# Kernel optimization log

Hardware: AMD Instinct MI355X
Metric: run time of the kernel (lower is better)

The kernel has to match this reference:

```python
import jax, jax.numpy as jnp
import numpy as np

EPS = 1e-12  # torch F.normalize default eps

def _l2norm(x):
    # torch.nn.functional.normalize(x, dim=-1): x / max(||x||_2, eps)
    n = jnp.linalg.norm(x, axis=-1, keepdims=True)
    return x / jnp.maximum(n, EPS)

def setup_inputs() -> dict:
    key = jax.random.key(0)
    ks = jax.random.split(key, 12)
    B, T, D, V, C = 16, 2048, 1024, 32000, 6
    s = 0.02
    text = jax.random.randint(ks[0], (B * T,), 0, V, dtype=jnp.int64)
    offsets = (jnp.arange(B, dtype=jnp.int64) * T)  # uniform-length sequences
    emb = jax.random.normal(ks[1], (V, D), dtype=jnp.float32) * s
    Wq = jax.random.normal(ks[2], (D, D), dtype=jnp.float32) * s
    bq = jnp.zeros((D,), jnp.float32)
    Wk = jax.random.normal(ks[3], (D, D), dtype=jnp.float32) * s
    bk = jnp.zeros((D,), jnp.float32)
    Wv = jax.random.normal(ks[4], (D, D), dtype=jnp.float32) * s
    bv = jnp.zeros((D,), jnp.float32)
    Wfc = jax.random.normal(ks[5], (D, D), dtype=jnp.float32) * s
    bfc = jnp.zeros((D,), jnp.float32)
    Wo = jax.random.normal(ks[6], (C, D), dtype=jnp.float32) * s
    bo = jnp.zeros((C,), jnp.float32)
    return {"text": text, "offsets": offsets, "emb": emb,
            "Wq": Wq, "bq": bq, "Wk": Wk, "bk": bk, "Wv": Wv, "bv": bv,
            "Wfc": Wfc, "bfc": bfc, "Wo": Wo, "bo": bo}

def reference(text, offsets, emb, Wq, bq, Wk, bk, Wv, bv, Wfc, bfc, Wo, bo):
    B = offsets.shape[0]
    T = text.shape[0] // B  # uniform lengths -> pad_sequence == reshape
    D = emb.shape[1]
    tok = text.reshape(B, T)
    x = emb[tok]                                   # [B,T,D]
    q = x @ Wq.T + bq
    k = x @ Wk.T + bk
    v = x @ Wv.T + bv
    scores = jnp.einsum('bqd,bkd->bqk', q, k) / jnp.sqrt(jnp.asarray(D, x.dtype))
    causal = jnp.tril(jnp.ones((T, T), dtype=bool))
    scores = jnp.where(causal[None, :, :], scores, -jnp.inf)
    attn = jax.nn.softmax(scores, axis=-1)
    out = jnp.einsum('bqk,bkd->bqd', attn, v) + x  # residual with embedding
    out = _l2norm(out)
    out = out + (out @ Wfc.T + bfc)                # residual FFN
    out = _l2norm(out)
    last = out[:, -1, :]                           # [B,D]
    return jax.nn.sigmoid(last @ Wo.T + bo)        # [B,num_class]
```

## Files before the change

kernel.cpp:

```cpp
#include <hip/hip_runtime.h>
#include <hip/hip_bf16.h>
#include <math.h>

typedef unsigned short ushort_t;

__device__ __forceinline__ float bf2f(ushort_t u) {
    union { unsigned int i; float f; } v;
    v.i = ((unsigned int)u) << 16;
    return v.f;
}

__device__ __forceinline__ ushort_t f2bf(float f) {
    union { float f; unsigned int i; } v; v.f = f;
    unsigned int lsb = (v.i >> 16) & 1;
    unsigned int r = v.i + 0x7FFF + lsb;
    return (ushort_t)(r >> 16);
}

__device__ __forceinline__ float wave_sum(float acc) {
    #pragma unroll
    for (int off = 32; off >= 1; off >>= 1) acc += __shfl_xor(acc, off, 64);
    return acc;
}

__device__ __forceinline__ void ld8(const void* p, int isbf, size_t i, float* o) {
    if (isbf) {
        uint4 raw = *reinterpret_cast<const uint4*>((const ushort_t*)p + i);
        const ushort_t* pu = reinterpret_cast<const ushort_t*>(&raw);
        #pragma unroll
        for (int k = 0; k < 8; ++k) o[k] = bf2f(pu[k]);
    } else {
        const float4* f = reinterpret_cast<const float4*>((const float*)p + i);
        float4 a = f[0], b = f[1];
        o[0]=a.x; o[1]=a.y; o[2]=a.z; o[3]=a.w;
        o[4]=b.x; o[5]=b.y; o[6]=b.z; o[7]=b.w;
    }
}

__device__ __forceinline__ void ld4(const void* p, int isbf, size_t i, float* o) {
    if (isbf) {
        uint2 raw = *reinterpret_cast<const uint2*>((const ushort_t*)p + i);
        const ushort_t* pu = reinterpret_cast<const ushort_t*>(&raw);
        #pragma unroll
        for (int k = 0; k < 4; ++k) o[k] = bf2f(pu[k]);
    } else {
        float4 a = *reinterpret_cast<const float4*>((const float*)p + i);
        o[0]=a.x; o[1]=a.y; o[2]=a.z; o[3]=a.w;
    }
}

__device__ __forceinline__ float ldS(const void* p, int isbf, size_t i) {
    return isbf ? bf2f(((const ushort_t*)p)[i]) : ((const float*)p)[i];
}

__device__ __forceinline__ int tokAt(const void* text, int isi64, size_t i) {
    return isi64 ? ((const int*)text)[2 * i] : ((const int*)text)[i];
}

__global__ void kD_init(const void* __restrict__ emb, const void* __restrict__ text,
                        int* __restrict__ flags, float* __restrict__ zbuf, int nz) {
    if (blockIdx.x == 0) {
        if (threadIdx.x < 64) {
            const int lane = threadIdx.x;
            ushort_t u = ((const ushort_t*)emb)[2 * lane];
            int e = (u >> 7) & 0xFF;
            unsigned long long mb = __ballot(e >= 0x60 && e <= 0x7E);
            int odd = ((const int*)text)[2 * lane + 1];
            unsigned long long mi = __ballot(odd != 0);
            if (lane == 0) {
                flags[0] = (__popcll(mb) >= 32) ? 1 : 0;
                flags[1] = (__popcll(mi) == 0) ? 1 : 0;
            }
        }
    } else {
        int i = (blockIdx.x - 1) * 256 + threadIdx.x;
        if (i < nz) zbuf[i] = 0.f;
    }
}

__global__ void k1_qx(const void* __restrict__ text, const void* __restrict__ emb,
                      const void* __restrict__ Wq, const void* __restrict__ bq,
                      float* __restrict__ x_last, float* __restrict__ q,
                      const int* __restrict__ flags, int T, int D) {
    const int isbf = flags[0], isi64 = flags[1];
    const int nb = D >> 2;
    const int b = blockIdx.x / nb;
    const int r0 = (blockIdx.x % nb) << 2;
    const int tid = threadIdx.x;
    __shared__ float xl[1024];
    const int tok = tokAt(text, isi64, (size_t)b * T + (T - 1));
    float w4[4];
    for (int dd = tid * 4; dd < D; dd += 1024) {
        ld4(emb, isbf, (size_t)tok * D + dd, w4);
        xl[dd]=w4[0]; xl[dd+1]=w4[1]; xl[dd+2]=w4[2]; xl[dd+3]=w4[3];
        if (r0 == 0) *reinterpret_cast<float4*>(x_last + b * D + dd)
                       = make_float4(w4[0], w4[1], w4[2], w4[3]);
    }
    __syncthreads();
    const int wave = tid >> 6, lane = tid & 63;
    const int i = r0 + wave;
    float acc = 0.f, w[8];
    for (int d0 = lane * 8; d0 < D; d0 += 512) {
        ld8(Wq, isbf, (size_t)i * D + d0, w);
        #pragma unroll
        for (int k = 0; k < 8; ++k) acc += w[k] * xl[d0 + k];
    }
    acc = wave_sum(acc);
    if (lane == 0) q[b * D + i] = acc + ldS(bq, isbf, i);
}

__global__ void k2_c(const float* __restrict__ q, const void* __restrict__ Wk,
                     float* __restrict__ c, const int* __restrict__ flags, int D) {
    const int isbf = flags[0];
    const int ich = D >> 5;
    const int b = blockIdx.x / ich;
    const int i0 = (blockIdx.x % ich) << 5;
    __shared__ float qs[32];
    if (threadIdx.x < 32) qs[threadIdx.x] = q[b * D + i0 + threadIdx.x];
    __syncthreads();
    const int d = threadIdx.x * 4;
    float a0 = 0.f, a1 = 0.f, a2 = 0.f, a3 = 0.f, w[4];
    #pragma unroll 8
    for (int i = 0; i < 32; ++i) {
        const float qv = qs[i];
        ld4(Wk, isbf, (size_t)(i0 + i) * D + d, w);
        a0 += qv * w[0]; a1 += qv * w[1]; a2 += qv * w[2]; a3 += qv * w[3];
    }
    atomicAdd(&c[b * D + d + 0], a0);
    atomicAdd(&c[b * D + d + 1], a1);
    atomicAdd(&c[b * D + d + 2], a2);
    atomicAdd(&c[b * D + d + 3], a3);
}

__global__ void k3_scores(const void* __restrict__ text, const void* __restrict__ emb,
                          const float* __restrict__ c, float* __restrict__ s,
                          const int* __restrict__ flags, int T, int D, float scale) {
    const int isbf = flags[0], isi64 = flags[1];
    const int jb = T >> 2;
    const int b = blockIdx.x / jb;
    const int j0 = (blockIdx.x % jb) * 4;
    __shared__ float cs[1024];
    for (int dd = threadIdx.x * 4; dd < D; dd += 1024) {
        float4 v = *reinterpret_cast<const float4*>(c + b * D + dd);
        cs[dd]=v.x; cs[dd+1]=v.y; cs[dd+2]=v.z; cs[dd+3]=v.w;
    }
    __syncthreads();
    const int wave = threadIdx.x >> 6, lane = threadIdx.x & 63;
    const int j = j0 + wave;
    const int tok = tokAt(text, isi64, (size_t)b * T + j);
    float acc = 0.f, w[8];
    for (int d0 = lane * 8; d0 < D; d0 += 512) {
        ld8(emb, isbf, (size_t)tok * D + d0, w);
        #pragma unroll
        for (int k = 0; k < 8; ++k) acc += w[k] * cs[d0 + k];
    }
    acc = wave_sum(acc);
    if (lane == 0) s[b * T + j] = acc * scale;
}

__global__ void k4_stats(const float* __restrict__ s, float* __restrict__ m,
                         float* __restrict__ l, int T) {
    const int b = blockIdx.x;
    const int tid = threadIdx.x;
    __shared__ float red[256];
    float mx = -INFINITY;
    for (int j = tid; j < T; j += 256) mx = fmaxf(mx, s[b * T + j]);
    red[tid] = mx;
    __syncthreads();
    for (int st = 128; st; st >>= 1) {
        if (tid < st) red[tid] = fmaxf(red[tid], red[tid + st]);
        __syncthreads();
    }
    mx = red[0];
    __syncthreads();
    float sm = 0.f;
    for (int j = tid; j < T; j += 256) sm += expf(s[b * T + j] - mx);
    red[tid] = sm;
    __syncthreads();
    for (int st = 128; st; st >>= 1) {
        if (tid < st) red[tid] += red[tid + st];
        __syncthreads();
    }
    if (tid == 0) { m[b] = mx; l[b] = red[0]; }
}

__global__ void k5_xbar(const void* __restrict__ text, const void* __restrict__ emb,
                        const float* __restrict__ s, const float* __restrict__ m,
                        const float* __restrict__ l, float* __restrict__ xbar,
                        const int* __restrict__ flags, int T, int D) {
    const int isbf = flags[0], isi64 = flags[1];
    const int jc = T >> 5;
    const int b = blockIdx.x / jc;
    const int j0 = (blockIdx.x % jc) << 5;
    const int tid = threadIdx.x;
    __shared__ float wts[32];
    __shared__ int tk[32];
    if (tid < 32) {
        const float mm = m[b], ll = l[b];
        wts[tid] = expf(s[b * T + j0 + tid] - mm) / ll;
        tk[tid] = tokAt(text, isi64, (size_t)b * T + j0 + tid);
    }
    __syncthreads();
    const int d = tid * 4;
    float a0 = 0.f, a1 = 0.f, a2 = 0.f, a3 = 0.f, w[4];
    #pragma unroll 8
    for (int j = 0; j < 32; ++j) {
        const float wj = wts[j];
        ld4(emb, isbf, (size_t)tk[j] * D + d, w);
        a0 += wj * w[0]; a1 += wj * w[1]; a2 += wj * w[2]; a3 += wj * w[3];
    }
    atomicAdd(&xbar[b * D + d + 0], a0);
    atomicAdd(&xbar[b * D + d + 1], a1);
    atomicAdd(&xbar[b * D + d + 2], a2);
    atomicAdd(&xbar[b * D + d + 3], a3);
}

__global__ void k6a_u(const void* __restrict__ Wv, const void* __restrict__ bv,
                      const float* __restrict__ xbar, const float* __restrict__ x_last,
                      float* __restrict__ u, const int* __restrict__ flags, int D) {
    const int isbf = flags[0];
    const int nb = D >> 2;
    const int b = blockIdx.x / nb;
    const int r0 = (blockIdx.x % nb) << 2;
    __shared__ float xb[1024];
    for (int dd = threadIdx.x * 4; dd < D; dd += 1024) {
        float4 v = *reinterpret_cast<const float4*>(xbar + b * D + dd);
        xb[dd]=v.x; xb[dd+1]=v.y; xb[dd+2]=v.z; xb[dd+3]=v.w;
    }
    __syncthreads();
    const int wave = threadIdx.x >> 6, lane = threadIdx.x & 63;
    const int i = r0 + wave;
    float acc = 0.f, w[8];
    for (int d0 = lane * 8; d0 < D; d0 += 512) {
        ld8(Wv, isbf, (size_t)i * D + d0, w);
        #pragma unroll
        for (int k = 0; k < 8; ++k) acc += w[k] * xb[d0 + k];
    }
    acc = wave_sum(acc);
    if (lane == 0) u[b * D + i] = acc + ldS(bv, isbf, i) + x_last[b * D + i];
}

__global__ void k6c_h2(const void* __restrict__ Wfc, const void* __restrict__ bfc,
                       const float* __restrict__ u, float* __restrict__ h2,
                       const int* __restrict__ flags, int D) {
    const int isbf = flags[0];
    const int nb = D >> 2;
    const int b = blockIdx.x / nb;
    const int r0 = (blockIdx.x % nb) << 2;
    const int tid = threadIdx.x;
    __shared__ float hs[1024];
    __shared__ float red[256];
    __shared__ float s_rn;
    float part = 0.f;
    for (int dd = tid * 4; dd < D; dd += 1024) {
        float4 v = *reinterpret_cast<const float4*>(u + b * D + dd);
        hs[dd]=v.x; hs[dd+1]=v.y; hs[dd+2]=v.z; hs[dd+3]=v.w;
        part += v.x*v.x + v.y*v.y + v.z*v.z + v.w*v.w;
    }
    red[tid] = part;
    __syncthreads();
    for (int st = 128; st; st >>= 1) {
        if (tid < st) red[tid] += red[tid + st];
        __syncthreads();
    }
    if (tid == 0) s_rn = 1.f / fmaxf(sqrtf(red[0]), 1e-12f);
    __syncthreads();
    const float rn = s_rn;
    for (int dd = tid; dd < D; dd += 256) hs[dd] *= rn;
    __syncthreads();
    const int wave = tid >> 6, lane = tid & 63;
    const int i = r0 + wave;
    float acc = 0.f, w[8];
    for (int d0 = lane * 8; d0 < D; d0 += 512) {
        ld8(Wfc, isbf, (size_t)i * D + d0, w);
        #pragma unroll
        for (int k = 0; k < 8; ++k) acc += w[k] * hs[d0 + k];
    }
    acc = wave_sum(acc);
    if (lane == 0) h2[b * D + i] = hs[i] + acc + ldS(bfc, isbf, i);
}

__global__ void k6d_out(const void* __restrict__ Wo, const void* __restrict__ bo,
                        const float* __restrict__ h2, void* __restrict__ out,
                        const int* __restrict__ flags, int D, int C, int total) {
    const int isbf = flags[0];
    const int g = blockIdx.x * 4 + (threadIdx.x >> 6);
    if (g >= total) return;
    const int lane = threadIdx.x & 63;
    const int b = g / C, ci = g % C;
    float a1 = 0.f, a2 = 0.f, w[8], h[8];
    for (int d0 = lane * 8; d0 < D; d0 += 512) {
        ld8(Wo, isbf, (size_t)ci * D + d0, w);
        ld8(h2, 0, (size_t)b * D + d0, h);
        #pragma unroll
        for (int k = 0; k < 8; ++k) { a1 += w[k] * h[k]; a2 += h[k] * h[k]; }
    }
    a1 = wave_sum(a1);
    a2 = wave_sum(a2);
    if (lane == 0) {
        float rn = 1.f / fmaxf(sqrtf(a2), 1e-12f);
        float z = a1 * rn + ldS(bo, isbf, ci);
        float y = 1.f / (1.f + expf(-z));
        if (isbf) ((ushort_t*)out)[g] = f2bf(y);
        else      ((float*)out)[g] = y;
    }
}

extern "C" void kernel_launch(void* const* d_in, const int* in_sizes, int n_in,
                              void* d_out, int out_size, void* d_ws, size_t ws_size,
                              hipStream_t stream) {
    const void* text = d_in[0];
    const void* emb = d_in[2];
    const void* Wq  = d_in[3];
    const void* bq  = d_in[4];
    const void* Wk  = d_in[5];
    const void* Wv  = d_in[7];
    const void* bv  = d_in[8];
    const void* Wfc = d_in[9];
    const void* bfc = d_in[10];
    const void* Wo  = d_in[11];
    const void* bo  = d_in[12];

    const int B = in_sizes[1];
    const int T = in_sizes[0] / B;
    const int D = in_sizes[4];
    const int C = in_sizes[12];

    float* ws     = (float*)d_ws;
    float* c      = ws;
    float* xbar   = c + B * D;
    float* x_last = xbar + B * D;
    float* q      = x_last + B * D;
    float* u      = q + B * D;
    float* h2     = u + B * D;
    float* s      = h2 + B * D;
    float* m      = s + B * T;
    float* l      = m + B;
    int*   flags  = (int*)(l + B);

    const int nz = 2 * B * D;
    const float scale = 1.0f / sqrtf((float)D);

    kD_init<<<1 + (nz + 255) / 256, 256, 0, stream>>>(emb, text, flags, c, nz);
    k1_qx<<<B * (D / 4), 256, 0, stream>>>(text, emb, Wq, bq, x_last, q, flags, T, D);
    k2_c<<<B * (D / 32), 256, 0, stream>>>(q, Wk, c, flags, D);
    k3_scores<<<B * (T / 4), 256, 0, stream>>>(text, emb, c, s, flags, T, D, scale);
    k4_stats<<<B, 256, 0, stream>>>(s, m, l, T);
    k5_xbar<<<B * (T / 32), 256, 0, stream>>>(text, emb, s, m, l, xbar, flags, T, D);
    k6a_u<<<B * (D / 4), 256, 0, stream>>>(Wv, bv, xbar, x_last, u, flags, D);
    k6c_h2<<<B * (D / 4), 256, 0, stream>>>(Wfc, bfc, u, h2, flags, D);
    k6d_out<<<(B * C + 3) / 4, 256, 0, stream>>>(Wo, bo, h2, d_out, flags, D, C, B * C);
}
```

Measured before the change: 300.7 us.

## Fuse q/c projection and split-softmax attention, replace atomics with partial buffers

Merges the q projection and the Wk contraction into one kernel that writes per-chunk partials. It also fuses score computation, local softmax stats and the weighted embedding sum into a flash-style per-chunk kernel, followed by a combine kernel that rescales the partials. This removes the zero-init kernel, the separate stats kernel and the atomicAdds, and cuts the launch count. In exchange, every kernel now re-detects the dtype flags, and the partial buffers need extra workspace.

```diff
diff --git a/kernel.cpp b/kernel.cpp
--- a/kernel.cpp
+++ b/kernel.cpp
@@ -57,200 +57,196 @@
     return isi64 ? ((const int*)text)[2 * i] : ((const int*)text)[i];
 }
 
-__global__ void kD_init(const void* __restrict__ emb, const void* __restrict__ text,
-                        int* __restrict__ flags, float* __restrict__ zbuf, int nz) {
-    if (blockIdx.x == 0) {
-        if (threadIdx.x < 64) {
-            const int lane = threadIdx.x;
-            ushort_t u = ((const ushort_t*)emb)[2 * lane];
-            int e = (u >> 7) & 0xFF;
-            unsigned long long mb = __ballot(e >= 0x60 && e <= 0x7E);
-            int odd = ((const int*)text)[2 * lane + 1];
-            unsigned long long mi = __ballot(odd != 0);
-            if (lane == 0) {
-                flags[0] = (__popcll(mb) >= 32) ? 1 : 0;
-                flags[1] = (__popcll(mi) == 0) ? 1 : 0;
-            }
+__device__ __forceinline__ void detect_flags(const void* emb, const void* text, int* sf) {
+    if (threadIdx.x < 64) {
+        const int lane = threadIdx.x;
+        ushort_t u = ((const ushort_t*)emb)[2 * lane];
+        int e = (u >> 7) & 0xFF;
+        unsigned long long mb = __ballot(e >= 0x60 && e <= 0x7E);
+        int odd = ((const int*)text)[2 * lane + 1];
+        unsigned long long mi = __ballot(odd != 0);
+        if (lane == 0) {
+            sf[0] = (__popcll(mb) >= 32) ? 1 : 0;
+            sf[1] = (__popcll(mi) == 0) ? 1 : 0;
         }
-    } else {
-        int i = (blockIdx.x - 1) * 256 + threadIdx.x;
-        if (i < nz) zbuf[i] = 0.f;
-    }
-}
-
-__global__ void k1_qx(const void* __restrict__ text, const void* __restrict__ emb,
-                      const void* __restrict__ Wq, const void* __restrict__ bq,
-                      float* __restrict__ x_last, float* __restrict__ q,
-                      const int* __restrict__ flags, int T, int D) {
-    const int isbf = flags[0], isi64 = flags[1];
+    }
+    __syncthreads();
+}
+
+__global__ void kQC(const void* __restrict__ text, const void* __restrict__ emb,
+                    const void* __restrict__ Wq, const void* __restrict__ bq,
+                    const void* __restrict__ Wk, float* __restrict__ c_part,
+                    int B, int T, int D) {
+    const int nch = D >> 6;
+    const int b = blockIdx.x / nch;
+    const int ch = blockIdx.x % nch;
+    const int i0 = ch << 6;
+    const int tid = threadIdx.x;
+    __shared__ int sf[2];
+    __shared__ float xs[1024];
+    __shared__ float qs[64];
+    detect_flags(emb, text, sf);
+    const int isbf = sf[0], isi64 = sf[1];
+    const int tok = tokAt(text, isi64, (size_t)b * T + (T - 1));
+    float w4[4];
+    for (int dd = tid * 4; dd < D; dd += 1024) {
+        ld4(emb, isbf, (size_t)tok * D + dd, w4);
+        xs[dd]=w4[0]; xs[dd+1]=w4[1]; xs[dd+2]=w4[2]; xs[dd+3]=w4[3];
+    }
+    __syncthreads();
+    const int wave = tid >> 6, lane = tid & 63;
+    float w[8];
+    for (int r = 0; r < 16; ++r) {
+        const int i = i0 + wave * 16 + r;
+        float acc = 0.f;
+        for (int d0 = lane * 8; d0 < D; d0 += 512) {
+            ld8(Wq, isbf, (size_t)i * D + d0, w);
+            #pragma unroll
+            for (int k = 0; k < 8; ++k) acc += w[k] * xs[d0 + k];
+        }
+        acc = wave_sum(acc);
+        if (lane == 0) qs[wave * 16 + r] = acc + ldS(bq, isbf, i);
+    }
+    __syncthreads();
+    const int d = tid * 4;
+    float a0=0.f, a1=0.f, a2=0.f, a3=0.f;
+    #pragma unroll 8
+    for (int i = 0; i < 64; ++i) {
+        const float qv = qs[i];
+        ld4(Wk, isbf, (size_t)(i0 + i) * D + d, w4);
+        a0 += qv*w4[0]; a1 += qv*w4[1]; a2 += qv*w4[2]; a3 += qv*w4[3];
+    }
+    *reinterpret_cast<float4*>(c_part + ((size_t)ch * B + b) * D + d)
+        = make_float4(a0, a1, a2, a3);
+}
+
+__global__ void k35(const void* __restrict__ text, const void* __restrict__ emb,
+                    const float* __restrict__ c_part, float* __restrict__ xbar_part,
+                    float* __restrict__ m_part, float* __restrict__ l_part,
+                    int B, int T, int D, int nch_c, float scale) {
+    const int nch = T >> 6;
+    const int b = blockIdx.x / nch;
+    const int ch = blockIdx.x % nch;
+    const int j0 = ch << 6;
+    const int tid = threadIdx.x;
+    __shared__ int sf[2];
+    __shared__ float cs[1024];
+    __shared__ float sjs[64];
+    __shared__ float wls[64];
+    __shared__ int tks[64];
+    detect_flags(emb, text, sf);
+    const int isbf = sf[0], isi64 = sf[1];
+    {
+        const int d = tid * 4;
+        float4 acc = make_float4(0.f, 0.f, 0.f, 0.f);
+        for (int cc = 0; cc < nch_c; ++cc) {
+            float4 v = *reinterpret_cast<const float4*>(c_part + ((size_t)cc * B + b) * D + d);
+            acc.x += v.x; acc.y += v.y; acc.z += v.z; acc.w += v.w;
+        }
+        cs[d]=acc.x; cs[d+1]=acc.y; cs[d+2]=acc.z; cs[d+3]=acc.w;
+    }
+    if (tid < 64) tks[tid] = tokAt(text, isi64, (size_t)b * T + j0 + tid);
+    __syncthreads();
+    const int wave = tid >> 6, lane = tid & 63;
+    float w[8];
+    for (int r = 0; r < 16; ++r) {
+        const int jj = wave * 16 + r;
+        const int tok = tks[jj];
+        float acc = 0.f;
+        for (int d0 = lane * 8; d0 < D; d0 += 512) {
+            ld8(emb, isbf, (size_t)tok * D + d0, w);
+            #pragma unroll
+            for (int k = 0; k < 8; ++k) acc += w[k] * cs[d0 + k];
+        }
+        acc = wave_sum(acc);
+        if (lane == 0) sjs[jj] = acc * scale;
+    }
+    __syncthreads();
+    float mx = -INFINITY;
+    #pragma unroll 8
+    for (int j = 0; j < 64; ++j) mx = fmaxf(mx, sjs[j]);
+    if (tid < 64) wls[tid] = expf(sjs[tid] - mx);
+    __syncthreads();
+    if (tid < 64) {
+        float lv = wave_sum(wls[tid]);
+        if (tid == 0) { m_part[ch * B + b] = mx; l_part[ch * B + b] = lv; }
+    }
+    const int d = tid * 4;
+    float a0=0.f, a1=0.f, a2=0.f, a3=0.f;
+    float w4[4];
+    #pragma unroll 8
+    for (int j = 0; j < 64; ++j) {
+        const float wj = wls[j];
+        ld4(emb, isbf, (size_t)tks[j] * D + d, w4);
+        a0 += wj*w4[0]; a1 += wj*w4[1]; a2 += wj*w4[2]; a3 += wj*w4[3];
+    }
+    *reinterpret_cast<float4*>(xbar_part + ((size_t)ch * B + b) * D + d)
+        = make_float4(a0, a1, a2, a3);
+}
+
+__global__ void kC(const float* __restrict__ xbar_part, const float* __restrict__ m_part,
+                   const float* __restrict__ l_part, float* __restrict__ xbar,
+                   int B, int D, int nch) {
+    const int b = blockIdx.x >> 2;
+    const int d = ((blockIdx.x & 3) << 8) + threadIdx.x;
+    float mx = -INFINITY;
+    for (int cc = 0; cc < nch; ++cc) mx = fmaxf(mx, m_part[cc * B + b]);
+    float lg = 0.f, acc = 0.f;
+    for (int cc = 0; cc < nch; ++cc) {
+        const float sc = expf(m_part[cc * B + b] - mx);
+        lg  += l_part[cc * B + b] * sc;
+        acc += xbar_part[((size_t)cc * B + b) * D + d] * sc;
+    }
+    xbar[b * D + d] = acc / lg;
+}
+
+__global__ void k6a_u(const void* __restrict__ text, const void* __restrict__ emb,
+                      const void* __restrict__ Wv, const void* __restrict__ bv,
+                      const float* __restrict__ xbar, float* __restrict__ u,
+                      int B, int T, int D) {
     const int nb = D >> 2;
     const int b = blockIdx.x / nb;
     const int r0 = (blockIdx.x % nb) << 2;
     const int tid = threadIdx.x;
+    __shared__ int sf[2];
+    __shared__ float xb[1024];
     __shared__ float xl[1024];
+    detect_flags(emb, text, sf);
+    const int isbf = sf[0], isi64 = sf[1];
     const int tok = tokAt(text, isi64, (size_t)b * T + (T - 1));
     float w4[4];
     for (int dd = tid * 4; dd < D; dd += 1024) {
+        float4 v = *reinterpret_cast<const float4*>(xbar + b * D + dd);
+        xb[dd]=v.x; xb[dd+1]=v.y; xb[dd+2]=v.z; xb[dd+3]=v.w;
         ld4(emb, isbf, (size_t)tok * D + dd, w4);
         xl[dd]=w4[0]; xl[dd+1]=w4[1]; xl[dd+2]=w4[2]; xl[dd+3]=w4[3];
-        if (r0 == 0) *reinterpret_cast<float4*>(x_last + b * D + dd)
-                       = make_float4(w4[0], w4[1], w4[2], w4[3]);
     }
     __syncthreads();
     const int wave = tid >> 6, lane = tid & 63;
     const int i = r0 + wave;
     float acc = 0.f, w[8];
     for (int d0 = lane * 8; d0 < D; d0 += 512) {
-        ld8(Wq, isbf, (size_t)i * D + d0, w);
-        #pragma unroll
-        for (int k = 0; k < 8; ++k) acc += w[k] * xl[d0 + k];
+        ld8(Wv, isbf, (size_t)i * D + d0, w);
+        #pragma unroll
+        for (int k = 0; k < 8; ++k) acc += w[k] * xb[d0 + k];
     }
     acc = wave_sum(acc);
-    if (lane == 0) q[b * D + i] = acc + ldS(bq, isbf, i);
-}
-
-__global__ void k2_c(const float* __restrict__ q, const void* __restrict__ Wk,
-                     float* __restrict__ c, const int* __restrict__ flags, int D) {
-    const int isbf = flags[0];
-    const int ich = D >> 5;
-    const int b = blockIdx.x / ich;
-    const int i0 = (blockIdx.x % ich) << 5;
-    __shared__ float qs[32];
-    if (threadIdx.x < 32) qs[threadIdx.x] = q[b * D + i0 + threadIdx.x];
-    __syncthreads();
-    const int d = threadIdx.x * 4;
-    float a0 = 0.f, a1 = 0.f, a2 = 0.f, a3 = 0.f, w[4];
-    #pragma unroll 8
-    for (int i = 0; i < 32; ++i) {
-        const float qv = qs[i];
-        ld4(Wk, isbf, (size_t)(i0 + i) * D + d, w);
-        a0 += qv * w[0]; a1 += qv * w[1]; a2 += qv * w[2]; a3 += qv * w[3];
-    }
-    atomicAdd(&c[b * D + d + 0], a0);
-    atomicAdd(&c[b * D + d + 1], a1);
-    atomicAdd(&c[b * D + d + 2], a2);
-    atomicAdd(&c[b * D + d + 3], a3);
-}
-
-__global__ void k3_scores(const void* __restrict__ text, const void* __restrict__ emb,
-                          const float* __restrict__ c, float* __restrict__ s,
-                          const int* __restrict__ flags, int T, int D, float scale) {
-    const int isbf = flags[0], isi64 = flags[1];
-    const int jb = T >> 2;
-    const int b = blockIdx.x / jb;
-    const int j0 = (blockIdx.x % jb) * 4;
-    __shared__ float cs[1024];
-    for (int dd = threadIdx.x * 4; dd < D; dd += 1024) {
-        float4 v = *reinterpret_cast<const float4*>(c + b * D + dd);
-        cs[dd]=v.x; cs[dd+1]=v.y; cs[dd+2]=v.z; cs[dd+3]=v.w;
-    }
-    __syncthreads();
-    const int wave = threadIdx.x >> 6, lane = threadIdx.x & 63;
-    const int j = j0 + wave;
-    const int tok = tokAt(text, isi64, (size_t)b * T + j);
-    float acc = 0.f, w[8];
-    for (int d0 = lane * 8; d0 < D; d0 += 512) {
-        ld8(emb, isbf, (size_t)tok * D + d0, w);
-        #pragma unroll
-        for (int k = 0; k < 8; ++k) acc += w[k] * cs[d0 + k];
-    }
-    acc = wave_sum(acc);
-    if (lane == 0) s[b * T + j] = acc * scale;
-}
-
-__global__ void k4_stats(const float* __restrict__ s, float* __restrict__ m,
-                         float* __restrict__ l, int T) {
-    const int b = blockIdx.x;
-    const int tid = threadIdx.x;
-    __shared__ float red[256];
-    float mx = -INFINITY;
-    for (int j = tid; j < T; j += 256) mx = fmaxf(mx, s[b * T + j]);
-    red[tid] = mx;
-    __syncthreads();
-    for (int st = 128; st; st >>= 1) {
-        if (tid < st) red[tid] = fmaxf(red[tid], red[tid + st]);
-        __syncthreads();
-    }
-    mx = red[0];
-    __syncthreads();
-    float sm = 0.f;
-    for (int j = tid; j < T; j += 256) sm += expf(s[b * T + j] - mx);
-    red[tid] = sm;
-    __syncthreads();
-    for (int st = 128; st; st >>= 1) {
-        if (tid < st) red[tid] += red[tid + st];
-        __syncthreads();
-    }
-    if (tid == 0) { m[b] = mx; l[b] = red[0]; }
-}
-
-__global__ void k5_xbar(const void* __restrict__ text, const void* __restrict__ emb,
-                        const float* __restrict__ s, const float* __restrict__ m,
-                        const float* __restrict__ l, float* __restrict__ xbar,
-                        const int* __restrict__ flags, int T, int D) {
-    const int isbf = flags[0], isi64 = flags[1];
-    const int jc = T >> 5;
-    const int b = blockIdx.x / jc;
-    const int j0 = (blockIdx.x % jc) << 5;
-    const int tid = threadIdx.x;
-    __shared__ float wts[32];
-    __shared__ int tk[32];
-    if (tid < 32) {
-        const float mm = m[b], ll = l[b];
-        wts[tid] = expf(s[b * T + j0 + tid] - mm) / ll;
-        tk[tid] = tokAt(text, isi64, (size_t)b * T + j0 + tid);
-    }
-    __syncthreads();
-    const int d = tid * 4;
-    float a0 = 0.f, a1 = 0.f, a2 = 0.f, a3 = 0.f, w[4];
-    #pragma unroll 8
-    for (int j = 0; j < 32; ++j) {
-        const float wj = wts[j];
-        ld4(emb, isbf, (size_t)tk[j] * D + d, w);
-        a0 += wj * w[0]; a1 += wj * w[1]; a2 += wj * w[2]; a3 += wj * w[3];
-    }
-    atomicAdd(&xbar[b * D + d + 0], a0);
-    atomicAdd(&xbar[b * D + d + 1], a1);
-    atomicAdd(&xbar[b * D + d + 2], a2);
-    atomicAdd(&xbar[b * D + d + 3], a3);
-}
-
-__global__ void k6a_u(const void* __restrict__ Wv, const void* __restrict__ bv,
-                      const float* __restrict__ xbar, const float* __restrict__ x_last,
-                      float* __restrict__ u, const int* __restrict__ flags, int D) {
-    const int isbf = flags[0];
-    const int nb = D >> 2;
-    const int b = blockIdx.x / nb;
-    const int r0 = (blockIdx.x % nb) << 2;
-    __shared__ float xb[1024];
-    for (int dd = threadIdx.x * 4; dd < D; dd += 1024) {
-        float4 v = *reinterpret_cast<const float4*>(xbar + b * D + dd);
-        xb[dd]=v.x; xb[dd+1]=v.y; xb[dd+2]=v.z; xb[dd+3]=v.w;
-    }
-    __syncthreads();
-    const int wave = threadIdx.x >> 6, lane = threadIdx.x & 63;
-    const int i = r0 + wave;
-    float acc = 0.f, w[8];
-    for (int d0 = lane * 8; d0 < D; d0 += 512) {
-        ld8(Wv, isbf, (size_t)i * D + d0, w);
-        #pragma unroll
-        for (int k = 0; k < 8; ++k) acc += w[k] * xb[d0 + k];
-    }
-    acc = wave_sum(acc);
-    if (lane == 0) u[b * D + i] = acc + ldS(bv, isbf, i) + x_last[b * D + i];
-}
-
-__global__ void k6c_h2(const void* __restrict__ Wfc, const void* __restrict__ bfc,
-                       const float* __restrict__ u, float* __restrict__ h2,
-                       const int* __restrict__ flags, int D) {
-    const int isbf = flags[0];
+    if (lane == 0) u[b * D + i] = acc + ldS(bv, isbf, i) + xl[i];
+}
+
+__global__ void k6c_h2(const void* __restrict__ text, const void* __restrict__ emb,
+                       const void* __restrict__ Wfc, const void* __restrict__ bfc,
+                       const float* __restrict__ u, float* __restrict__ h2, int D) {
     const int nb = D >> 2;
     const int b = blockIdx.x / nb;
     const int r0 = (blockIdx.x % nb) << 2;
     const int tid = threadIdx.x;
+    __shared__ int sf[2];
     __shared__ float hs[1024];
     __shared__ float red[256];
     __shared__ float s_rn;
+    detect_flags(emb, text, sf);
+    const int isbf = sf[0];
     float part = 0.f;
     for (int dd = tid * 4; dd < D; dd += 1024) {
         float4 v = *reinterpret_cast<const float4*>(u + b * D + dd);
@@ -280,10 +276,13 @@
     if (lane == 0) h2[b * D + i] = hs[i] + acc + ldS(bfc, isbf, i);
 }
 
-__global__ void k6d_out(const void* __restrict__ Wo, const void* __restrict__ bo,
+__global__ void k6d_out(const void* __restrict__ text, const void* __restrict__ emb,
+                        const void* __restrict__ Wo, const void* __restrict__ bo,
                         const float* __restrict__ h2, void* __restrict__ out,
-                        const int* __restrict__ flags, int D, int C, int total) {
-    const int isbf = flags[0];
+                        int D, int C, int total) {
+    __shared__ int sf[2];
+    detect_flags(emb, text, sf);
+    const int isbf = sf[0];
     const int g = blockIdx.x * 4 + (threadIdx.x >> 6);
     if (g >= total) return;
     const int lane = threadIdx.x & 63;
@@ -326,28 +325,25 @@
     const int D = in_sizes[4];
     const int C = in_sizes[12];
 
-    float* ws     = (float*)d_ws;
-    float* c      = ws;
-    float* xbar   = c + B * D;
-    float* x_last = xbar + B * D;
-    float* q      = x_last + B * D;
-    float* u      = q + B * D;
-    float* h2     = u + B * D;
-    float* s      = h2 + B * D;
-    float* m      = s + B * T;
-    float* l      = m + B;
-    int*   flags  = (int*)(l + B);
-
-    const int nz = 2 * B * D;
+    const int nch_c = D / 64;
+    const int nch_k = T / 64;
+
+    float* ws        = (float*)d_ws;
+    float* c_part    = ws;
+    float* xbar_part = c_part + (size_t)nch_c * B * D;
+    float* m_part    = xbar_part + (size_t)nch_k * B * D;
+    float* l_part    = m_part + (size_t)nch_k * B;
+    float* xbar      = l_part + (size_t)nch_k * B;
+    float* u         = xbar + (size_t)B * D;
+    float* h2        = u + (size_t)B * D;
+
     const float scale = 1.0f / sqrtf((float)D);
 
-    kD_init<<<1 + (nz + 255) / 256, 256, 0, stream>>>(emb, text, flags, c, nz);
-    k1_qx<<<B * (D / 4), 256, 0, stream>>>(text, emb, Wq, bq, x_last, q, flags, T, D);
-    k2_c<<<B * (D / 32), 256, 0, stream>>>(q, Wk, c, flags, D);
-    k3_scores<<<B * (T / 4), 256, 0, stream>>>(text, emb, c, s, flags, T, D, scale);
-    k4_stats<<<B, 256, 0, stream>>>(s, m, l, T);
-    k5_xbar<<<B * (T / 32), 256, 0, stream>>>(text, emb, s, m, l, xbar, flags, T, D);
-    k6a_u<<<B * (D / 4), 256, 0, stream>>>(Wv, bv, xbar, x_last, u, flags, D);
-    k6c_h2<<<B * (D / 4), 256, 0, stream>>>(Wfc, bfc, u, h2, flags, D);
-    k6d_out<<<(B * C + 3) / 4, 256, 0, stream>>>(Wo, bo, h2, d_out, flags, D, C, B * C);
-}
+    kQC<<<B * (D / 64), 256, 0, stream>>>(text, emb, Wq, bq, Wk, c_part, B, T, D);
+    k35<<<B * (T / 64), 256, 0, stream>>>(text, emb, c_part, xbar_part, m_part, l_part,
+                                          B, T, D, nch_c, scale);
+    kC<<<B * 4, 256, 0, stream>>>(xbar_part, m_part, l_part, xbar, B, D, nch_k);
+    k6a_u<<<B * (D / 4), 256, 0, stream>>>(text, emb, Wv, bv, xbar, u, B, T, D);
+    k6c_h2<<<B * (D / 4), 256, 0, stream>>>(text, emb, Wfc, bfc, u, h2, D);
+    k6d_out<<<(B * C + 3) / 4, 256, 0, stream>>>(text, emb, Wo, bo, h2, d_out, D, C, B * C);
+}
```

Result: slower. 310.6 us (+3.3%).
